# Performance work log

Measured on AMD Instinct MI355X. Metric: run time of the kernel, lower is better.

Reference implementation:

```python
import jax, jax.numpy as jnp
import numpy as np

B, T, C, H = 4096, 32, 180, 6
HD = C // H  # 30
EPS = 1e-5

def _ln(x, g, b):
    mu = jnp.mean(x, axis=-1, keepdims=True)
    var = jnp.mean(jnp.square(x - mu), axis=-1, keepdims=True)
    return (x - mu) * jax.lax.rsqrt(var + EPS) * g + b

def setup_inputs() -> dict:
    key = jax.random.key(0)
    ks = jax.random.split(key, 12)
    s_in = 1.0 / np.sqrt(C)
    s_ff = 1.0 / np.sqrt(4 * C)
    return {
        "x": jax.random.normal(ks[0], (B, T, C), jnp.float32),
        "wq": jax.random.normal(ks[1], (H, C, HD), jnp.float32) * s_in,
        "wk": jax.random.normal(ks[2], (H, C, HD), jnp.float32) * s_in,
        "wv": jax.random.normal(ks[3], (H, C, HD), jnp.float32) * s_in,
        "g1": jnp.ones((C,), jnp.float32),
        "be1": jnp.zeros((C,), jnp.float32),
        "g2": jnp.ones((C,), jnp.float32),
        "be2": jnp.zeros((C,), jnp.float32),
        "w1": jax.random.normal(ks[4], (C, 4 * C), jnp.float32) * s_in,
        "b1": jnp.zeros((4 * C,), jnp.float32),
        "w2": jax.random.normal(ks[5], (4 * C, C), jnp.float32) * s_ff,
        "b2": jnp.zeros((C,), jnp.float32),
    }

def reference(x, wq, wk, wv, g1, be1, g2, be2, w1, b1, w2, b2):
    Bv, Tv, Cv = x.shape
    h = _ln(x, g1, be1)
    # batched multi-head QKV (replaces per-head Python loop)
    q = jnp.einsum('btc,hcd->bhtd', h, wq)
    k = jnp.einsum('btc,hcd->bhtd', h, wk)
    v = jnp.einsum('btc,hcd->bhtd', h, wv)
    scores = jnp.einsum('bhtd,bhsd->bhts', q, k) * (HD ** -0.5)
    mask = jnp.tril(jnp.ones((Tv, Tv), bool))
    scores = jnp.where(mask, scores, -jnp.inf)
    attn = jax.nn.softmax(scores, axis=-1)  # dropout off (eval)
    out = jnp.einsum('bhts,bhsd->bhtd', attn, v)
    out = jnp.transpose(out, (0, 2, 1, 3)).reshape(Bv, Tv, Cv)  # concat heads
    x = x + out
    h2 = _ln(x, g2, be2)
    mlp = jax.nn.relu(h2 @ w1 + b1) @ w2 + b2  # dropout off (eval)
    return x + mlp
```

## Files before the change

kernel.cpp:

```cpp
#include <hip/hip_runtime.h>

typedef __attribute__((ext_vector_type(8))) short short8;
typedef __attribute__((ext_vector_type(4))) float f32x4;
typedef unsigned short ushort_t;
typedef unsigned int u32;
typedef unsigned long long u64;

#define MFMA16(a,b,c) __builtin_amdgcn_mfma_f32_16x16x32_bf16((a),(b),(c),0,0,0)

__device__ __forceinline__ ushort_t f2bf(float f){
  union { float f; u32 u; } v; v.f = f;
  u32 r = v.u + 0x7fffu + ((v.u >> 16) & 1u);
  return (ushort_t)(r >> 16);
}
__device__ __forceinline__ float bf2f(ushort_t h){
  union { u32 u; float f; } v; v.u = ((u32)h) << 16; return v.f;
}
__device__ __forceinline__ u64 pack4(float a, float b, float c, float d){
  u32 p0 = (u32)f2bf(a) | ((u32)f2bf(b) << 16);
  u32 p1 = (u32)f2bf(c) | ((u32)f2bf(d) << 16);
  return (u64)p0 | ((u64)p1 << 32);
}

template<int CTRL>
__device__ __forceinline__ float dpp_add(float x){
  union { float f; int i; } a, b;
  a.f = x;
  b.i = __builtin_amdgcn_update_dpp(a.i, a.i, CTRL, 0xF, 0xF, false);
  return x + b.f;
}
__device__ __forceinline__ float red4_add(float x){
  x = dpp_add<0xB1>(x); x = dpp_add<0x4E>(x);
  return x;
}

#define WQKV_ELEMS (576*192)
#define W1T_ELEMS  (768*192)
#define W2T_ELEMS  (192*768)

#define S64 208
#define SSC 44

__global__ void prep_weights(const float* __restrict__ wq, const float* __restrict__ wk,
                             const float* __restrict__ wv, const float* __restrict__ w1,
                             const float* __restrict__ w2, ushort_t* __restrict__ ws){
  ushort_t* wqkv = ws;
  ushort_t* w1t = ws + WQKV_ELEMS;
  ushort_t* w2t = w1t + W1T_ELEMS;
  int tid = blockIdx.x * blockDim.x + threadIdx.x;
  int stride = gridDim.x * blockDim.x;
  for (int i = tid; i < WQKV_ELEMS; i += stride){
    int k = i % 192; int row = i / 192;
    int d = row & 31; int m = (row >> 5) % 3; int h = row / 96;
    float v = 0.f;
    if (d < 30 && k < 180){
      const float* W = (m == 0) ? wq : ((m == 1) ? wk : wv);
      v = W[(h*180 + k)*30 + d];
    }
    wqkv[i] = f2bf(v);
  }
  for (int i = tid; i < W1T_ELEMS; i += stride){
    int c = i % 192; int n = i / 192;
    float v = (n < 720 && c < 180) ? w1[c*720 + n] : 0.f;
    w1t[i] = f2bf(v);
  }
  for (int i = tid; i < W2T_ELEMS; i += stride){
    int c4 = i % 768; int n = i / 768;
    float v = (n < 180 && c4 < 720) ? w2[c4*180 + n] : 0.f;
    w2t[i] = f2bf(v);
  }
}

union AttnU { ushort_t hx[64*S64]; ushort_t sc[4][2][32*SSC]; };

__global__ __launch_bounds__(256, 2)
void attn_kernel(const float* __restrict__ x, const float* __restrict__ g1,
                 const float* __restrict__ be1, const ushort_t* __restrict__ wqkv,
                 float* __restrict__ xout){
  __shared__ AttnU u;
  __shared__ ushort_t hn[64*S64];
  __shared__ ushort_t att[64*S64];

  int tid = threadIdx.x;
  int wave = tid >> 6, lane = tid & 63;
  int quad = lane >> 4, c16 = lane & 15;
  long base = (long)blockIdx.x * 11520;

  #pragma unroll
  for (int it = 0; it < 12; it++){
    int idx = it*256 + tid;
    if (idx < 2880){
      f32x4 v = *(const f32x4*)(x + base + (long)idx*4);
      int row = (int)(((u32)idx * 745655u) >> 25);
      int col = idx - row*45;
      *(u64*)(u.hx + row*S64 + col*4) = pack4(v.x, v.y, v.z, v.w);
    } else {
      int p = idx - 2880;
      int row = (p*21846) >> 16;
      int g = p - row*3;
      *(u64*)(u.hx + row*S64 + 180 + g*4) = 0ull;
    }
  }
  __syncthreads();

  {
    int row = tid >> 2, sub = tid & 3;
    int c0 = sub*48;
    float s1 = 0.f, s2 = 0.f;
    #pragma unroll
    for (int gi = 0; gi < 12; gi++){
      u64 m = *(const u64*)(u.hx + row*S64 + c0 + gi*4);
      #pragma unroll
      for (int e = 0; e < 4; e++){
        float v = bf2f((ushort_t)(m >> (16*e)));
        s1 += v; s2 += v*v;
      }
    }
    s1 = red4_add(s1); s2 = red4_add(s2);
    float mu = s1 * (1.f/180.f);
    float rstd = rsqrtf(s2 * (1.f/180.f) - mu*mu + 1e-5f);
    #pragma unroll
    for (int gi = 0; gi < 12; gi++){
      int c = c0 + gi*4;
      if (c < 180){
        u64 m = *(const u64*)(u.hx + row*S64 + c);
        f32x4 g = *(const f32x4*)(g1 + c);
        f32x4 be = *(const f32x4*)(be1 + c);
        float v0 = (bf2f((ushort_t)(m    )) - mu)*rstd*g.x + be.x;
        float v1 = (bf2f((ushort_t)(m>>16)) - mu)*rstd*g.y + be.y;
        float v2 = (bf2f((ushort_t)(m>>32)) - mu)*rstd*g.z + be.z;
        float v3 = (bf2f((ushort_t)(m>>48)) - mu)*rstd*g.w + be.w;
        *(u64*)(hn + row*S64 + c) = pack4(v0, v1, v2, v3);
      } else {
        *(u64*)(hn + row*S64 + c) = 0ull;
      }
    }
  }
  __syncthreads();

  {
    int bb = wave >> 1;
    ushort_t* buf0 = u.sc[wave][0];
    ushort_t* buf1 = u.sc[wave][1];
    const float scl = 0.18257418583505537f;

    for (int hh = 0; hh < 3; hh++){
      int head = (wave & 1)*3 + hh;
      const ushort_t* wbase = wqkv + head*96*192;

      short8 aqw[2][6], akw[2][6];
      #pragma unroll
      for (int mt = 0; mt < 2; mt++)
        #pragma unroll
        for (int kk = 0; kk < 6; kk++){
          aqw[mt][kk] = *(const short8*)(wbase + (      mt*16 + c16)*192 + kk*32 + quad*8);
          akw[mt][kk] = *(const short8*)(wbase + (32  + mt*16 + c16)*192 + kk*32 + quad*8);
        }

      f32x4 accq[2][2], acck[2][2], accv[2][2];
      #pragma unroll
      for (int i = 0; i < 2; i++)
        #pragma unroll
        for (int j = 0; j < 2; j++){ accq[i][j]=(f32x4)0.f; acck[i][j]=(f32x4)0.f; accv[i][j]=(f32x4)0.f; }

      #pragma unroll
      for (int kk = 0; kk < 6; kk++){
        short8 hf[2];
        #pragma unroll
        for (int nt = 0; nt < 2; nt++)
          hf[nt] = *(const short8*)(hn + (bb*32 + nt*16 + c16)*S64 + kk*32 + quad*8);
        short8 avw[2];
        #pragma unroll
        for (int nt = 0; nt < 2; nt++)
          avw[nt] = *(const short8*)(wbase + (64 + nt*16 + c16)*192 + kk*32 + quad*8);
        #pragma unroll
        for (int mt = 0; mt < 2; mt++)
          #pragma unroll
          for (int nt = 0; nt < 2; nt++){
            accq[mt][nt] = MFMA16(aqw[mt][kk], hf[nt], accq[mt][nt]);
            acck[mt][nt] = MFMA16(akw[mt][kk], hf[nt], acck[mt][nt]);
            accv[mt][nt] = MFMA16(hf[mt], avw[nt], accv[mt][nt]);
          }
      }
      #pragma unroll
      for (int mt = 0; mt < 2; mt++)
        #pragma unroll
        for (int nt = 0; nt < 2; nt++){
          *(u64*)(buf0 + (nt*16 + c16)*SSC + mt*16 + quad*4) =
            pack4(accq[mt][nt][0], accq[mt][nt][1], accq[mt][nt][2], accq[mt][nt][3]);
          *(u64*)(buf1 + (nt*16 + c16)*SSC + mt*16 + quad*4) =
            pack4(acck[mt][nt][0], acck[mt][nt][1], acck[mt][nt][2], acck[mt][nt][3]);
        }
      f32x4 sacc[2][2];
      #pragma unroll
      for (int i = 0; i < 2; i++){ sacc[i][0]=(f32x4)0.f; sacc[i][1]=(f32x4)0.f; }
      short8 ak[2], bq[2];
      #pragma unroll
      for (int mt = 0; mt < 2; mt++) ak[mt] = *(const short8*)(buf1 + (mt*16 + c16)*SSC + quad*8);
      #pragma unroll
      for (int nt = 0; nt < 2; nt++) bq[nt] = *(const short8*)(buf0 + (nt*16 + c16)*SSC + quad*8);
      #pragma unroll
      for (int mt = 0; mt < 2; mt++)
        #pragma unroll
        for (int nt = 0; nt < 2; nt++)
          sacc[mt][nt] = MFMA16(ak[mt], bq[nt], sacc[mt][nt]);
      #pragma unroll
      for (int nt = 0; nt < 2; nt++){
        int t = nt*16 + c16;
        float v[8];
        #pragma unroll
        for (int r = 0; r < 4; r++){
          int s0 = quad*4 + r, s1v = 16 + quad*4 + r;
          v[r]   = (s0  > t) ? -1e30f : sacc[0][nt][r]*scl;
          v[4+r] = (s1v > t) ? -1e30f : sacc[1][nt][r]*scl;
        }
        float m = v[0];
        #pragma unroll
        for (int i = 1; i < 8; i++) m = fmaxf(m, v[i]);
        m = fmaxf(m, __shfl_xor(m, 16));
        m = fmaxf(m, __shfl_xor(m, 32));
        float e[8], s = 0.f;
        #pragma unroll
        for (int i = 0; i < 8; i++){ e[i] = __expf(v[i] - m); s += e[i]; }
        s += __shfl_xor(s, 16);
        s += __shfl_xor(s, 32);
        float inv = 1.f / s;
        *(u64*)(buf1 + t*SSC +      quad*4) = pack4(e[0]*inv, e[1]*inv, e[2]*inv, e[3]*inv);
        *(u64*)(buf1 + t*SSC + 16 + quad*4) = pack4(e[4]*inv, e[5]*inv, e[6]*inv, e[7]*inv);
      }
      #pragma unroll
      for (int mt = 0; mt < 2; mt++)
        #pragma unroll
        for (int nt = 0; nt < 2; nt++)
          *(u64*)(buf0 + (nt*16 + c16)*SSC + mt*16 + quad*4) =
            pack4(accv[mt][nt][0], accv[mt][nt][1], accv[mt][nt][2], accv[mt][nt][3]);
      f32x4 oacc[2][2];
      #pragma unroll
      for (int i = 0; i < 2; i++){ oacc[i][0]=(f32x4)0.f; oacc[i][1]=(f32x4)0.f; }
      short8 av[2], bp[2];
      #pragma unroll
      for (int mt = 0; mt < 2; mt++) av[mt] = *(const short8*)(buf0 + (mt*16 + c16)*SSC + quad*8);
      #pragma unroll
      for (int nt = 0; nt < 2; nt++) bp[nt] = *(const short8*)(buf1 + (nt*16 + c16)*SSC + quad*8);
      #pragma unroll
      for (int mt = 0; mt < 2; mt++)
        #pragma unroll
        for (int nt = 0; nt < 2; nt++)
          oacc[mt][nt] = MFMA16(av[mt], bp[nt], oacc[mt][nt]);
      #pragma unroll
      for (int mt = 0; mt < 2; mt++)
        #pragma unroll
        for (int nt = 0; nt < 2; nt++)
          *(u64*)(att + (bb*32 + nt*16 + c16)*S64 + head*32 + mt*16 + quad*4) =
            pack4(oacc[mt][nt][0], oacc[mt][nt][1], oacc[mt][nt][2], oacc[mt][nt][3]);
    }
  }
  __syncthreads();

  #pragma unroll
  for (int it = 0; it < 12; it++){
    int idx = it*256 + tid;
    if (idx < 2880){
      f32x4 v = *(const f32x4*)(x + base + (long)idx*4);
      int row = (int)(((u32)idx * 745655u) >> 25);
      int col4 = (idx - row*45)*4;
      #pragma unroll
      for (int e = 0; e < 4; e++){
        int c = col4 + e;
        int h = (c*4370) >> 17;
        int d = c - h*30;
        v[e] += bf2f(att[row*S64 + h*32 + d]);
      }
      *(f32x4*)(xout + base + (long)idx*4) = v;
    }
  }
}

union MlpU { ushort_t hx[64*S64]; };

__global__ __launch_bounds__(256, 2)
void mlp_kernel(const float* __restrict__ g2, const float* __restrict__ be2,
                const float* __restrict__ b1, const float* __restrict__ b2,
                const ushort_t* __restrict__ w1t, const ushort_t* __restrict__ w2t,
                float* __restrict__ xio){
  __shared__ MlpU u;
  __shared__ ushort_t hn[64*S64];
  int tid = threadIdx.x;
  int wave = tid >> 6, lane = tid & 63;
  int quad = lane >> 4, c16 = lane & 15;
  long base = (long)blockIdx.x * 11520;

  #pragma unroll
  for (int it = 0; it < 12; it++){
    int idx = it*256 + tid;
    if (idx < 2880){
      f32x4 v = *(const f32x4*)(xio + base + (long)idx*4);
      int row = (int)(((u32)idx * 745655u) >> 25);
      int col = idx - row*45;
      *(u64*)(u.hx + row*S64 + col*4) = pack4(v.x, v.y, v.z, v.w);
    } else {
      int p = idx - 2880;
      int row = (p*21846) >> 16;
      int g = p - row*3;
      *(u64*)(u.hx + row*S64 + 180 + g*4) = 0ull;
    }
  }
  __syncthreads();

  {
    int row = tid >> 2, sub = tid & 3;
    int c0 = sub*48;
    float s1 = 0.f, s2 = 0.f;
    #pragma unroll
    for (int gi = 0; gi < 12; gi++){
      u64 m = *(const u64*)(u.hx + row*S64 + c0 + gi*4);
      #pragma unroll
      for (int e = 0; e < 4; e++){
        float v = bf2f((ushort_t)(m >> (16*e)));
        s1 += v; s2 += v*v;
      }
    }
    s1 = red4_add(s1); s2 = red4_add(s2);
    float mu = s1 * (1.f/180.f);
    float rstd = rsqrtf(s2 * (1.f/180.f) - mu*mu + 1e-5f);
    #pragma unroll
    for (int gi = 0; gi < 12; gi++){
      int c = c0 + gi*4;
      if (c < 180){
        u64 m = *(const u64*)(u.hx + row*S64 + c);
        f32x4 g = *(const f32x4*)(g2 + c);
        f32x4 be = *(const f32x4*)(be2 + c);
        float v0 = (bf2f((ushort_t)(m    )) - mu)*rstd*g.x + be.x;
        float v1 = (bf2f((ushort_t)(m>>16)) - mu)*rstd*g.y + be.y;
        float v2 = (bf2f((ushort_t)(m>>32)) - mu)*rstd*g.z + be.z;
        float v3 = (bf2f((ushort_t)(m>>48)) - mu)*rstd*g.w + be.w;
        *(u64*)(hn + row*S64 + c) = pack4(v0, v1, v2, v3);
      } else {
        *(u64*)(hn + row*S64 + c) = 0ull;
      }
    }
  }
  __syncthreads();

  ushort_t* act = u.hx;
  f32x4 outacc[3][4];
  #pragma unroll
  for (int i = 0; i < 3; i++)
    #pragma unroll
    for (int j = 0; j < 4; j++) outacc[i][j] = (f32x4)0.f;

  for (int ch = 0; ch < 4; ch++){
    short8 aw[3][6];
    #pragma unroll
    for (int mi = 0; mi < 3; mi++)
      #pragma unroll
      for (int kk = 0; kk < 6; kk++)
        aw[mi][kk] = *(const short8*)(w1t + (size_t)(ch*192 + (wave*3+mi)*16 + c16)*192 + kk*32 + quad*8);

    f32x4 aacc[3][4];
    #pragma unroll
    for (int i = 0; i < 3; i++)
      #pragma unroll
      for (int j = 0; j < 4; j++) aacc[i][j] = (f32x4)0.f;
    #pragma unroll
    for (int kk = 0; kk < 6; kk++){
      short8 bh[4];
      #pragma unroll
      for (int tt = 0; tt < 4; tt++)
        bh[tt] = *(const short8*)(hn + (tt*16 + c16)*S64 + kk*32 + quad*8);
      #pragma unroll
      for (int mi = 0; mi < 3; mi++)
        #pragma unroll
        for (int tt = 0; tt < 4; tt++)
          aacc[mi][tt] = MFMA16(aw[mi][kk], bh[tt], aacc[mi][tt]);
    }
    __syncthreads();
    #pragma unroll
    for (int mi = 0; mi < 3; mi++){
      int nrel = (wave*3+mi)*16 + quad*4;
      int nabs = ch*192 + nrel;
      f32x4 bias = (f32x4)0.f;
      if (nabs < 720) bias = *(const f32x4*)(b1 + nabs);
      #pragma unroll
      for (int tt = 0; tt < 4; tt++){
        float v0 = fmaxf(aacc[mi][tt][0] + bias[0], 0.f);
        float v1 = fmaxf(aacc[mi][tt][1] + bias[1], 0.f);
        float v2 = fmaxf(aacc[mi][tt][2] + bias[2], 0.f);
        float v3 = fmaxf(aacc[mi][tt][3] + bias[3], 0.f);
        *(u64*)(act + (tt*16 + c16)*S64 + nrel) = pack4(v0, v1, v2, v3);
      }
    }
    __syncthreads();

    short8 bw[3][6];
    #pragma unroll
    for (int ntl = 0; ntl < 3; ntl++)
      #pragma unroll
      for (int kk = 0; kk < 6; kk++)
        bw[ntl][kk] = *(const short8*)(w2t + (size_t)(wave*48 + ntl*16 + c16)*768 + ch*192 + kk*32 + quad*8);

    #pragma unroll
    for (int kk = 0; kk < 6; kk++){
      short8 aa[4];
      #pragma unroll
      for (int tt = 0; tt < 4; tt++)
        aa[tt] = *(const short8*)(act + (tt*16 + c16)*S64 + kk*32 + quad*8);
      #pragma unroll
      for (int ntl = 0; ntl < 3; ntl++)
        #pragma unroll
        for (int tt = 0; tt < 4; tt++)
          outacc[ntl][tt] = MFMA16(bw[ntl][kk], aa[tt], outacc[ntl][tt]);
    }
  }
  __syncthreads();
  #pragma unroll
  for (int ntl = 0; ntl < 3; ntl++){
    int no = wave*48 + ntl*16 + quad*4;
    #pragma unroll
    for (int tt = 0; tt < 4; tt++)
      *(u64*)(act + (tt*16 + c16)*S64 + no) =
        pack4(outacc[ntl][tt][0], outacc[ntl][tt][1], outacc[ntl][tt][2], outacc[ntl][tt][3]);
  }
  __syncthreads();
  #pragma unroll
  for (int it = 0; it < 12; it++){
    int idx = it*256 + tid;
    if (idx < 2880){
      f32x4 v = *(const f32x4*)(xio + base + (long)idx*4);
      int row = (int)(((u32)idx * 745655u) >> 25);
      int col4 = (idx - row*45)*4;
      f32x4 bb = *(const f32x4*)(b2 + col4);
      u64 m = *(const u64*)(act + row*S64 + col4);
      v.x += bf2f((ushort_t)(m      )) + bb.x;
      v.y += bf2f((ushort_t)(m >> 16)) + bb.y;
      v.z += bf2f((ushort_t)(m >> 32)) + bb.z;
      v.w += bf2f((ushort_t)(m >> 48)) + bb.w;
      *(f32x4*)(xio + base + (long)idx*4) = v;
    }
  }
}

extern "C" void kernel_launch(void* const* d_in, const int* in_sizes, int n_in,
                              void* d_out, int out_size, void* d_ws, size_t ws_size,
                              hipStream_t stream) {
  const float* x   = (const float*)d_in[0];
  const float* wq  = (const float*)d_in[1];
  const float* wk  = (const float*)d_in[2];
  const float* wv  = (const float*)d_in[3];
  const float* g1  = (const float*)d_in[4];
  const float* be1 = (const float*)d_in[5];
  const float* g2  = (const float*)d_in[6];
  const float* be2 = (const float*)d_in[7];
  const float* w1  = (const float*)d_in[8];
  const float* b1  = (const float*)d_in[9];
  const float* w2  = (const float*)d_in[10];
  const float* b2  = (const float*)d_in[11];
  ushort_t* ws   = (ushort_t*)d_ws;
  ushort_t* wqkv = ws;
  ushort_t* w1t  = ws + WQKV_ELEMS;
  ushort_t* w2t  = w1t + W1T_ELEMS;
  float* out = (float*)d_out;

  prep_weights<<<256, 256, 0, stream>>>(wq, wk, wv, w1, w2, ws);
  attn_kernel<<<2048, 256, 0, stream>>>(x, g1, be1, wqkv, out);
  mlp_kernel<<<2048, 256, 0, stream>>>(g2, be2, b1, b2, w1t, w2t, out);
}
```

Baseline: 493.3 us.

## Fuse attention and MLP into one kernel with one sequence per block

```diff
diff --git a/kernel.cpp b/kernel.cpp
--- a/kernel.cpp
+++ b/kernel.cpp
@@ -38,8 +38,9 @@
 #define W1T_ELEMS  (768*192)
 #define W2T_ELEMS  (192*768)
 
-#define S64 208
-#define SSC 44
+#define SH 200
+#define SS 40
+#define SA 196
 
 __global__ void prep_weights(const float* __restrict__ wq, const float* __restrict__ wk,
                              const float* __restrict__ wv, const float* __restrict__ w1,
@@ -71,139 +72,134 @@
   }
 }
 
-union AttnU { ushort_t hx[64*S64]; ushort_t sc[4][2][32*SSC]; };
-
-__global__ __launch_bounds__(256, 2)
-void attn_kernel(const float* __restrict__ x, const float* __restrict__ g1,
-                 const float* __restrict__ be1, const ushort_t* __restrict__ wqkv,
-                 float* __restrict__ xout){
-  __shared__ AttnU u;
-  __shared__ ushort_t hn[64*S64];
-  __shared__ ushort_t att[64*S64];
+__global__ __launch_bounds__(256, 4)
+void block_kernel(const float* __restrict__ x,
+                  const float* __restrict__ g1, const float* __restrict__ be1,
+                  const float* __restrict__ g2, const float* __restrict__ be2,
+                  const float* __restrict__ b1, const float* __restrict__ b2,
+                  const ushort_t* __restrict__ wqkv, const ushort_t* __restrict__ w1t,
+                  const ushort_t* __restrict__ w2t, float* __restrict__ out){
+  __shared__ __align__(16) ushort_t regA[7680];
+  __shared__ __align__(16) ushort_t hn[32*SH];
+  __shared__ __align__(16) ushort_t att[32*SA];
 
   int tid = threadIdx.x;
   int wave = tid >> 6, lane = tid & 63;
   int quad = lane >> 4, c16 = lane & 15;
-  long base = (long)blockIdx.x * 11520;
+  long base = (long)blockIdx.x * 5760;
 
   #pragma unroll
-  for (int it = 0; it < 12; it++){
+  for (int it = 0; it < 6; it++){
     int idx = it*256 + tid;
-    if (idx < 2880){
+    if (idx < 1440){
       f32x4 v = *(const f32x4*)(x + base + (long)idx*4);
       int row = (int)(((u32)idx * 745655u) >> 25);
       int col = idx - row*45;
-      *(u64*)(u.hx + row*S64 + col*4) = pack4(v.x, v.y, v.z, v.w);
+      *(u64*)(regA + row*SH + col*4) = pack4(v.x, v.y, v.z, v.w);
     } else {
-      int p = idx - 2880;
+      int p = idx - 1440;
       int row = (p*21846) >> 16;
       int g = p - row*3;
-      *(u64*)(u.hx + row*S64 + 180 + g*4) = 0ull;
+      *(u64*)(regA + row*SH + 180 + g*4) = 0ull;
     }
   }
   __syncthreads();
 
   {
-    int row = tid >> 2, sub = tid & 3;
-    int c0 = sub*48;
+    int row = tid >> 3, sub = tid & 7;
+    int c0 = sub*24;
     float s1 = 0.f, s2 = 0.f;
     #pragma unroll
-    for (int gi = 0; gi < 12; gi++){
-      u64 m = *(const u64*)(u.hx + row*S64 + c0 + gi*4);
+    for (int gi = 0; gi < 6; gi++){
+      u64 m = *(const u64*)(regA + row*SH + c0 + gi*4);
       #pragma unroll
       for (int e = 0; e < 4; e++){
         float v = bf2f((ushort_t)(m >> (16*e)));
         s1 += v; s2 += v*v;
       }
     }
-    s1 = red4_add(s1); s2 = red4_add(s2);
+    s1 = red4_add(s1); s1 += __shfl_xor(s1, 4);
+    s2 = red4_add(s2); s2 += __shfl_xor(s2, 4);
     float mu = s1 * (1.f/180.f);
     float rstd = rsqrtf(s2 * (1.f/180.f) - mu*mu + 1e-5f);
     #pragma unroll
-    for (int gi = 0; gi < 12; gi++){
+    for (int gi = 0; gi < 6; gi++){
       int c = c0 + gi*4;
       if (c < 180){
-        u64 m = *(const u64*)(u.hx + row*S64 + c);
+        u64 m = *(const u64*)(regA + row*SH + c);
         f32x4 g = *(const f32x4*)(g1 + c);
         f32x4 be = *(const f32x4*)(be1 + c);
         float v0 = (bf2f((ushort_t)(m    )) - mu)*rstd*g.x + be.x;
         float v1 = (bf2f((ushort_t)(m>>16)) - mu)*rstd*g.y + be.y;
         float v2 = (bf2f((ushort_t)(m>>32)) - mu)*rstd*g.z + be.z;
         float v3 = (bf2f((ushort_t)(m>>48)) - mu)*rstd*g.w + be.w;
-        *(u64*)(hn + row*S64 + c) = pack4(v0, v1, v2, v3);
+        *(u64*)(hn + row*SH + c) = pack4(v0, v1, v2, v3);
       } else {
-        *(u64*)(hn + row*S64 + c) = 0ull;
-      }
-    }
-  }
-  __syncthreads();
-
-  {
-    int bb = wave >> 1;
-    ushort_t* buf0 = u.sc[wave][0];
-    ushort_t* buf1 = u.sc[wave][1];
+        *(u64*)(hn + row*SH + c) = 0ull;
+      }
+    }
+  }
+  __syncthreads();
+
+  if (wave < 3){
+    ushort_t* buf0 = regA + wave*2560;
+    ushort_t* buf1 = buf0 + 32*SS;
     const float scl = 0.18257418583505537f;
 
-    for (int hh = 0; hh < 3; hh++){
-      int head = (wave & 1)*3 + hh;
-      const ushort_t* wbase = wqkv + head*96*192;
-
-      short8 aqw[2][6], akw[2][6];
-      #pragma unroll
-      for (int mt = 0; mt < 2; mt++)
-        #pragma unroll
-        for (int kk = 0; kk < 6; kk++){
-          aqw[mt][kk] = *(const short8*)(wbase + (      mt*16 + c16)*192 + kk*32 + quad*8);
-          akw[mt][kk] = *(const short8*)(wbase + (32  + mt*16 + c16)*192 + kk*32 + quad*8);
+    #pragma unroll
+    for (int hh = 0; hh < 2; hh++){
+      int head = wave*2 + hh;
+      const ushort_t* wbase = wqkv + head*(96*192);
+
+      f32x4 accq[2][2], acck[2][2], accv[2][2];
+      #pragma unroll
+      for (int i = 0; i < 2; i++)
+        #pragma unroll
+        for (int j = 0; j < 2; j++){ accq[i][j]=(f32x4)0.f; acck[i][j]=(f32x4)0.f; accv[i][j]=(f32x4)0.f; }
+
+      #pragma unroll
+      for (int kk = 0; kk < 6; kk++){
+        short8 hf[2], aq[2], ak[2], av[2];
+        #pragma unroll
+        for (int nt = 0; nt < 2; nt++)
+          hf[nt] = *(const short8*)(hn + (nt*16 + c16)*SH + kk*32 + quad*8);
+        #pragma unroll
+        for (int mt = 0; mt < 2; mt++){
+          aq[mt] = *(const short8*)(wbase + (      mt*16 + c16)*192 + kk*32 + quad*8);
+          ak[mt] = *(const short8*)(wbase + (32  + mt*16 + c16)*192 + kk*32 + quad*8);
+          av[mt] = *(const short8*)(wbase + (64  + mt*16 + c16)*192 + kk*32 + quad*8);
         }
-
-      f32x4 accq[2][2], acck[2][2], accv[2][2];
-      #pragma unroll
-      for (int i = 0; i < 2; i++)
-        #pragma unroll
-        for (int j = 0; j < 2; j++){ accq[i][j]=(f32x4)0.f; acck[i][j]=(f32x4)0.f; accv[i][j]=(f32x4)0.f; }
-
-      #pragma unroll
-      for (int kk = 0; kk < 6; kk++){
-        short8 hf[2];
-        #pragma unroll
-        for (int nt = 0; nt < 2; nt++)
-          hf[nt] = *(const short8*)(hn + (bb*32 + nt*16 + c16)*S64 + kk*32 + quad*8);
-        short8 avw[2];
-        #pragma unroll
-        for (int nt = 0; nt < 2; nt++)
-          avw[nt] = *(const short8*)(wbase + (64 + nt*16 + c16)*192 + kk*32 + quad*8);
         #pragma unroll
         for (int mt = 0; mt < 2; mt++)
           #pragma unroll
           for (int nt = 0; nt < 2; nt++){
-            accq[mt][nt] = MFMA16(aqw[mt][kk], hf[nt], accq[mt][nt]);
-            acck[mt][nt] = MFMA16(akw[mt][kk], hf[nt], acck[mt][nt]);
-            accv[mt][nt] = MFMA16(hf[mt], avw[nt], accv[mt][nt]);
+            accq[mt][nt] = MFMA16(aq[mt], hf[nt], accq[mt][nt]);
+            acck[mt][nt] = MFMA16(ak[mt], hf[nt], acck[mt][nt]);
+            accv[mt][nt] = MFMA16(hf[mt], av[nt], accv[mt][nt]);
           }
       }
       #pragma unroll
       for (int mt = 0; mt < 2; mt++)
         #pragma unroll
         for (int nt = 0; nt < 2; nt++){
-          *(u64*)(buf0 + (nt*16 + c16)*SSC + mt*16 + quad*4) =
+          *(u64*)(buf0 + (nt*16 + c16)*SS + mt*16 + quad*4) =
             pack4(accq[mt][nt][0], accq[mt][nt][1], accq[mt][nt][2], accq[mt][nt][3]);
-          *(u64*)(buf1 + (nt*16 + c16)*SSC + mt*16 + quad*4) =
+          *(u64*)(buf1 + (nt*16 + c16)*SS + mt*16 + quad*4) =
             pack4(acck[mt][nt][0], acck[mt][nt][1], acck[mt][nt][2], acck[mt][nt][3]);
         }
       f32x4 sacc[2][2];
       #pragma unroll
       for (int i = 0; i < 2; i++){ sacc[i][0]=(f32x4)0.f; sacc[i][1]=(f32x4)0.f; }
-      short8 ak[2], bq[2];
-      #pragma unroll
-      for (int mt = 0; mt < 2; mt++) ak[mt] = *(const short8*)(buf1 + (mt*16 + c16)*SSC + quad*8);
-      #pragma unroll
-      for (int nt = 0; nt < 2; nt++) bq[nt] = *(const short8*)(buf0 + (nt*16 + c16)*SSC + quad*8);
+      short8 akf[2], bqf[2];
+      #pragma unroll
+      for (int mt = 0; mt < 2; mt++) akf[mt] = *(const short8*)(buf1 + (mt*16 + c16)*SS + quad*8);
+      #pragma unroll
+      for (int nt = 0; nt < 2; nt++) bqf[nt] = *(const short8*)(buf0 + (nt*16 + c16)*SS + quad*8);
       #pragma unroll
       for (int mt = 0; mt < 2; mt++)
         #pragma unroll
         for (int nt = 0; nt < 2; nt++)
-          sacc[mt][nt] = MFMA16(ak[mt], bq[nt], sacc[mt][nt]);
+          sacc[mt][nt] = MFMA16(akf[mt], bqf[nt], sacc[mt][nt]);
       #pragma unroll
       for (int nt = 0; nt < 2; nt++){
         int t = nt*16 + c16;
@@ -225,42 +221,42 @@
         s += __shfl_xor(s, 16);
         s += __shfl_xor(s, 32);
         float inv = 1.f / s;
-        *(u64*)(buf1 + t*SSC +      quad*4) = pack4(e[0]*inv, e[1]*inv, e[2]*inv, e[3]*inv);
-        *(u64*)(buf1 + t*SSC + 16 + quad*4) = pack4(e[4]*inv, e[5]*inv, e[6]*inv, e[7]*inv);
+        *(u64*)(buf1 + t*SS +      quad*4) = pack4(e[0]*inv, e[1]*inv, e[2]*inv, e[3]*inv);
+        *(u64*)(buf1 + t*SS + 16 + quad*4) = pack4(e[4]*inv, e[5]*inv, e[6]*inv, e[7]*inv);
       }
       #pragma unroll
       for (int mt = 0; mt < 2; mt++)
         #pragma unroll
         for (int nt = 0; nt < 2; nt++)
-          *(u64*)(buf0 + (nt*16 + c16)*SSC + mt*16 + quad*4) =
+          *(u64*)(buf0 + (nt*16 + c16)*SS + mt*16 + quad*4) =
             pack4(accv[mt][nt][0], accv[mt][nt][1], accv[mt][nt][2], accv[mt][nt][3]);
       f32x4 oacc[2][2];
       #pragma unroll
       for (int i = 0; i < 2; i++){ oacc[i][0]=(f32x4)0.f; oacc[i][1]=(f32x4)0.f; }
-      short8 av[2], bp[2];
-      #pragma unroll
-      for (int mt = 0; mt < 2; mt++) av[mt] = *(const short8*)(buf0 + (mt*16 + c16)*SSC + quad*8);
-      #pragma unroll
-      for (int nt = 0; nt < 2; nt++) bp[nt] = *(const short8*)(buf1 + (nt*16 + c16)*SSC + quad*8);
+      short8 avf[2], bpf[2];
+      #pragma unroll
+      for (int mt = 0; mt < 2; mt++) avf[mt] = *(const short8*)(buf0 + (mt*16 + c16)*SS + quad*8);
+      #pragma unroll
+      for (int nt = 0; nt < 2; nt++) bpf[nt] = *(const short8*)(buf1 + (nt*16 + c16)*SS + quad*8);
       #pragma unroll
       for (int mt = 0; mt < 2; mt++)
         #pragma unroll
         for (int nt = 0; nt < 2; nt++)
-          oacc[mt][nt] = MFMA16(av[mt], bp[nt], oacc[mt][nt]);
+          oacc[mt][nt] = MFMA16(avf[mt], bpf[nt], oacc[mt][nt]);
       #pragma unroll
       for (int mt = 0; mt < 2; mt++)
         #pragma unroll
         for (int nt = 0; nt < 2; nt++)
-          *(u64*)(att + (bb*32 + nt*16 + c16)*S64 + head*32 + mt*16 + quad*4) =
+          *(u64*)(att + (nt*16 + c16)*SA + head*32 + mt*16 + quad*4) =
             pack4(oacc[mt][nt][0], oacc[mt][nt][1], oacc[mt][nt][2], oacc[mt][nt][3]);
     }
   }
   __syncthreads();
 
   #pragma unroll
-  for (int it = 0; it < 12; it++){
+  for (int it = 0; it < 6; it++){
     int idx = it*256 + tid;
-    if (idx < 2880){
+    if (idx < 1440){
       f32x4 v = *(const f32x4*)(x + base + (long)idx*4);
       int row = (int)(((u32)idx * 745655u) >> 25);
       int col4 = (idx - row*45)*4;
@@ -269,173 +265,146 @@
         int c = col4 + e;
         int h = (c*4370) >> 17;
         int d = c - h*30;
-        v[e] += bf2f(att[row*S64 + h*32 + d]);
-      }
-      *(f32x4*)(xout + base + (long)idx*4) = v;
-    }
-  }
-}
-
-union MlpU { ushort_t hx[64*S64]; };
-
-__global__ __launch_bounds__(256, 2)
-void mlp_kernel(const float* __restrict__ g2, const float* __restrict__ be2,
-                const float* __restrict__ b1, const float* __restrict__ b2,
-                const ushort_t* __restrict__ w1t, const ushort_t* __restrict__ w2t,
-                float* __restrict__ xio){
-  __shared__ MlpU u;
-  __shared__ ushort_t hn[64*S64];
-  int tid = threadIdx.x;
-  int wave = tid >> 6, lane = tid & 63;
-  int quad = lane >> 4, c16 = lane & 15;
-  long base = (long)blockIdx.x * 11520;
-
-  #pragma unroll
-  for (int it = 0; it < 12; it++){
-    int idx = it*256 + tid;
-    if (idx < 2880){
-      f32x4 v = *(const f32x4*)(xio + base + (long)idx*4);
-      int row = (int)(((u32)idx * 745655u) >> 25);
-      int col = idx - row*45;
-      *(u64*)(u.hx + row*S64 + col*4) = pack4(v.x, v.y, v.z, v.w);
+        v[e] += bf2f(att[row*SA + h*32 + d]);
+      }
+      *(u64*)(regA + row*SH + col4) = pack4(v.x, v.y, v.z, v.w);
     } else {
-      int p = idx - 2880;
+      int p = idx - 1440;
       int row = (p*21846) >> 16;
       int g = p - row*3;
-      *(u64*)(u.hx + row*S64 + 180 + g*4) = 0ull;
+      *(u64*)(regA + row*SH + 180 + g*4) = 0ull;
     }
   }
   __syncthreads();
 
   {
-    int row = tid >> 2, sub = tid & 3;
-    int c0 = sub*48;
+    int row = tid >> 3, sub = tid & 7;
+    int c0 = sub*24;
     float s1 = 0.f, s2 = 0.f;
     #pragma unroll
-    for (int gi = 0; gi < 12; gi++){
-      u64 m = *(const u64*)(u.hx + row*S64 + c0 + gi*4);
+    for (int gi = 0; gi < 6; gi++){
+      u64 m = *(const u64*)(regA + row*SH + c0 + gi*4);
       #pragma unroll
       for (int e = 0; e < 4; e++){
         float v = bf2f((ushort_t)(m >> (16*e)));
         s1 += v; s2 += v*v;
       }
     }
-    s1 = red4_add(s1); s2 = red4_add(s2);
+    s1 = red4_add(s1); s1 += __shfl_xor(s1, 4);
+    s2 = red4_add(s2); s2 += __shfl_xor(s2, 4);
     float mu = s1 * (1.f/180.f);
     float rstd = rsqrtf(s2 * (1.f/180.f) - mu*mu + 1e-5f);
     #pragma unroll
-    for (int gi = 0; gi < 12; gi++){
+    for (int gi = 0; gi < 6; gi++){
       int c = c0 + gi*4;
       if (c < 180){
-        u64 m = *(const u64*)(u.hx + row*S64 + c);
+        u64 m = *(const u64*)(regA + row*SH + c);
         f32x4 g = *(const f32x4*)(g2 + c);
         f32x4 be = *(const f32x4*)(be2 + c);
         float v0 = (bf2f((ushort_t)(m    )) - mu)*rstd*g.x + be.x;
         float v1 = (bf2f((ushort_t)(m>>16)) - mu)*rstd*g.y + be.y;
         float v2 = (bf2f((ushort_t)(m>>32)) - mu)*rstd*g.z + be.z;
         float v3 = (bf2f((ushort_t)(m>>48)) - mu)*rstd*g.w + be.w;
-        *(u64*)(hn + row*S64 + c) = pack4(v0, v1, v2, v3);
+        *(u64*)(hn + row*SH + c) = pack4(v0, v1, v2, v3);
       } else {
-        *(u64*)(hn + row*S64 + c) = 0ull;
-      }
-    }
-  }
-  __syncthreads();
-
-  ushort_t* act = u.hx;
-  f32x4 outacc[3][4];
+        *(u64*)(hn + row*SH + c) = 0ull;
+      }
+    }
+  }
+  __syncthreads();
+
+  {
+    ushort_t* act = regA;
+    f32x4 outacc[3][2];
+    #pragma unroll
+    for (int i = 0; i < 3; i++)
+      #pragma unroll
+      for (int j = 0; j < 2; j++) outacc[i][j] = (f32x4)0.f;
+
+    for (int ch = 0; ch < 4; ch++){
+      f32x4 aacc[3][2];
+      #pragma unroll
+      for (int i = 0; i < 3; i++)
+        #pragma unroll
+        for (int j = 0; j < 2; j++) aacc[i][j] = (f32x4)0.f;
+      #pragma unroll
+      for (int kk = 0; kk < 6; kk++){
+        short8 bh[2];
+        #pragma unroll
+        for (int tt = 0; tt < 2; tt++)
+          bh[tt] = *(const short8*)(hn + (tt*16 + c16)*SH + kk*32 + quad*8);
+        short8 aw[3];
+        #pragma unroll
+        for (int mi = 0; mi < 3; mi++)
+          aw[mi] = *(const short8*)(w1t + (size_t)(ch*192 + (wave*3+mi)*16 + c16)*192 + kk*32 + quad*8);
+        #pragma unroll
+        for (int mi = 0; mi < 3; mi++)
+          #pragma unroll
+          for (int tt = 0; tt < 2; tt++)
+            aacc[mi][tt] = MFMA16(aw[mi], bh[tt], aacc[mi][tt]);
+      }
+      __syncthreads();
+      #pragma unroll
+      for (int mi = 0; mi < 3; mi++){
+        int nrel = (wave*3+mi)*16 + quad*4;
+        int nabs = ch*192 + nrel;
+        f32x4 bias = (f32x4)0.f;
+        if (nabs < 720) bias = *(const f32x4*)(b1 + nabs);
+        #pragma unroll
+        for (int tt = 0; tt < 2; tt++){
+          float v0 = fmaxf(aacc[mi][tt][0] + bias[0], 0.f);
+          float v1 = fmaxf(aacc[mi][tt][1] + bias[1], 0.f);
+          float v2 = fmaxf(aacc[mi][tt][2] + bias[2], 0.f);
+          float v3 = fmaxf(aacc[mi][tt][3] + bias[3], 0.f);
+          *(u64*)(act + (tt*16 + c16)*SH + nrel) = pack4(v0, v1, v2, v3);
+        }
+      }
+      __syncthreads();
+      #pragma unroll
+      for (int kk = 0; kk < 6; kk++){
+        short8 aa[2];
+        #pragma unroll
+        for (int tt = 0; tt < 2; tt++)
+          aa[tt] = *(const short8*)(act + (tt*16 + c16)*SH + kk*32 + quad*8);
+        short8 bw[3];
+        #pragma unroll
+        for (int ntl = 0; ntl < 3; ntl++)
+          bw[ntl] = *(const short8*)(w2t + (size_t)(wave*48 + ntl*16 + c16)*768 + ch*192 + kk*32 + quad*8);
+        #pragma unroll
+        for (int ntl = 0; ntl < 3; ntl++)
+          #pragma unroll
+          for (int tt = 0; tt < 2; tt++)
+            outacc[ntl][tt] = MFMA16(bw[ntl], aa[tt], outacc[ntl][tt]);
+      }
+    }
+    #pragma unroll
+    for (int ntl = 0; ntl < 3; ntl++){
+      int no = wave*48 + ntl*16 + quad*4;
+      #pragma unroll
+      for (int tt = 0; tt < 2; tt++)
+        *(u64*)(hn + (tt*16 + c16)*SH + no) =
+          pack4(outacc[ntl][tt][0], outacc[ntl][tt][1], outacc[ntl][tt][2], outacc[ntl][tt][3]);
+    }
+  }
+  __syncthreads();
+
   #pragma unroll
-  for (int i = 0; i < 3; i++)
-    #pragma unroll
-    for (int j = 0; j < 4; j++) outacc[i][j] = (f32x4)0.f;
-
-  for (int ch = 0; ch < 4; ch++){
-    short8 aw[3][6];
-    #pragma unroll
-    for (int mi = 0; mi < 3; mi++)
-      #pragma unroll
-      for (int kk = 0; kk < 6; kk++)
-        aw[mi][kk] = *(const short8*)(w1t + (size_t)(ch*192 + (wave*3+mi)*16 + c16)*192 + kk*32 + quad*8);
-
-    f32x4 aacc[3][4];
-    #pragma unroll
-    for (int i = 0; i < 3; i++)
-      #pragma unroll
-      for (int j = 0; j < 4; j++) aacc[i][j] = (f32x4)0.f;
-    #pragma unroll
-    for (int kk = 0; kk < 6; kk++){
-      short8 bh[4];
-      #pragma unroll
-      for (int tt = 0; tt < 4; tt++)
-        bh[tt] = *(const short8*)(hn + (tt*16 + c16)*S64 + kk*32 + quad*8);
-      #pragma unroll
-      for (int mi = 0; mi < 3; mi++)
-        #pragma unroll
-        for (int tt = 0; tt < 4; tt++)
-          aacc[mi][tt] = MFMA16(aw[mi][kk], bh[tt], aacc[mi][tt]);
-    }
-    __syncthreads();
-    #pragma unroll
-    for (int mi = 0; mi < 3; mi++){
-      int nrel = (wave*3+mi)*16 + quad*4;
-      int nabs = ch*192 + nrel;
-      f32x4 bias = (f32x4)0.f;
-      if (nabs < 720) bias = *(const f32x4*)(b1 + nabs);
-      #pragma unroll
-      for (int tt = 0; tt < 4; tt++){
-        float v0 = fmaxf(aacc[mi][tt][0] + bias[0], 0.f);
-        float v1 = fmaxf(aacc[mi][tt][1] + bias[1], 0.f);
-        float v2 = fmaxf(aacc[mi][tt][2] + bias[2], 0.f);
-        float v3 = fmaxf(aacc[mi][tt][3] + bias[3], 0.f);
-        *(u64*)(act + (tt*16 + c16)*S64 + nrel) = pack4(v0, v1, v2, v3);
-      }
-    }
-    __syncthreads();
-
-    short8 bw[3][6];
-    #pragma unroll
-    for (int ntl = 0; ntl < 3; ntl++)
-      #pragma unroll
-      for (int kk = 0; kk < 6; kk++)
-        bw[ntl][kk] = *(const short8*)(w2t + (size_t)(wave*48 + ntl*16 + c16)*768 + ch*192 + kk*32 + quad*8);
-
-    #pragma unroll
-    for (int kk = 0; kk < 6; kk++){
-      short8 aa[4];
-      #pragma unroll
-      for (int tt = 0; tt < 4; tt++)
-        aa[tt] = *(const short8*)(act + (tt*16 + c16)*S64 + kk*32 + quad*8);
-      #pragma unroll
-      for (int ntl = 0; ntl < 3; ntl++)
-        #pragma unroll
-        for (int tt = 0; tt < 4; tt++)
-          outacc[ntl][tt] = MFMA16(bw[ntl][kk], aa[tt], outacc[ntl][tt]);
-    }
-  }
-  __syncthreads();
-  #pragma unroll
-  for (int ntl = 0; ntl < 3; ntl++){
-    int no = wave*48 + ntl*16 + quad*4;
-    #pragma unroll
-    for (int tt = 0; tt < 4; tt++)
-      *(u64*)(act + (tt*16 + c16)*S64 + no) =
-        pack4(outacc[ntl][tt][0], outacc[ntl][tt][1], outacc[ntl][tt][2], outacc[ntl][tt][3]);
-  }
-  __syncthreads();
-  #pragma unroll
-  for (int it = 0; it < 12; it++){
+  for (int it = 0; it < 6; it++){
     int idx = it*256 + tid;
-    if (idx < 2880){
-      f32x4 v = *(const f32x4*)(xio + base + (long)idx*4);
+    if (idx < 1440){
+      f32x4 v = *(const f32x4*)(x + base + (long)idx*4);
       int row = (int)(((u32)idx * 745655u) >> 25);
       int col4 = (idx - row*45)*4;
       f32x4 bb = *(const f32x4*)(b2 + col4);
-      u64 m = *(const u64*)(act + row*S64 + col4);
-      v.x += bf2f((ushort_t)(m      )) + bb.x;
-      v.y += bf2f((ushort_t)(m >> 16)) + bb.y;
-      v.z += bf2f((ushort_t)(m >> 32)) + bb.z;
-      v.w += bf2f((ushort_t)(m >> 48)) + bb.w;
-      *(f32x4*)(xio + base + (long)idx*4) = v;
+      u64 m = *(const u64*)(hn + row*SH + col4);
+      #pragma unroll
+      for (int e = 0; e < 4; e++){
+        int c = col4 + e;
+        int h = (c*4370) >> 17;
+        int d = c - h*30;
+        v[e] += bf2f(att[row*SA + h*32 + d]) + bf2f((ushort_t)(m >> (16*e))) + bb[e];
+      }
+      *(f32x4*)(out + base + (long)idx*4) = v;
     }
   }
 }
@@ -462,6 +431,6 @@
   float* out = (float*)d_out;
 
   prep_weights<<<256, 256, 0, stream>>>(wq, wk, wv, w1, w2, ws);
-  attn_kernel<<<2048, 256, 0, stream>>>(x, g1, be1, wqkv, out);
-  mlp_kernel<<<2048, 256, 0, stream>>>(g2, be2, b1, b2, w1t, w2t, out);
-}
+  block_kernel<<<4096, 256, 0, stream>>>(x, g1, be1, g2, be2, b1, b2,
+                                         wqkv, w1t, w2t, out);
+}
```

Result: slower. 566.0 us (+14.7%).
